# Optimization experiments

Measured on AMD Instinct MI355X. Metric: run time of the kernel, lower is better.

The kernel has to match this reference:

```python
import jax, jax.numpy as jnp
import numpy as np

N = 524288   # sparse points
C = 64       # io channels
AC = 128     # attn channels
H = 8        # heads
PS = 64      # patch size
HID = 256    # mlp hidden (mlp_ratio=2)
HD = AC // H # head dim
EPS = 1e-5


def _ln(x):
    mu = x.mean(-1, keepdims=True)
    v = x.var(-1, keepdims=True)
    return (x - mu) / jnp.sqrt(v + EPS)


def setup_inputs() -> dict:
    key = jax.random.key(0)
    ks = jax.random.split(key, 12)
    def w(k, shape, fan_in):
        return jax.random.normal(k, shape, jnp.float32) * (1.0 / np.sqrt(fan_in))
    return {
        "feats": jax.random.normal(ks[0], (N, C), jnp.float32),
        "w_pre": w(ks[1], (C, AC), C),    "b_pre": jnp.zeros((AC,), jnp.float32),
        "g1": jnp.ones((AC,), jnp.float32), "b1": jnp.zeros((AC,), jnp.float32),
        "w_qkv": w(ks[2], (AC, 3 * AC), AC), "b_qkv": jnp.zeros((3 * AC,), jnp.float32),
        "w_proj": w(ks[3], (AC, AC), AC), "b_proj": jnp.zeros((AC,), jnp.float32),
        "g2": jnp.ones((AC,), jnp.float32), "b2": jnp.zeros((AC,), jnp.float32),
        "w_m1": w(ks[4], (AC, HID), AC),  "b_m1": jnp.zeros((HID,), jnp.float32),
        "w_m2": w(ks[5], (HID, AC), HID), "b_m2": jnp.zeros((AC,), jnp.float32),
        "w_post": w(ks[6], (AC, C), AC),  "b_post": jnp.zeros((C,), jnp.float32),
    }


def reference(feats, w_pre, b_pre, g1, b1, w_qkv, b_qkv, w_proj, b_proj,
              g2, b2, w_m1, b_m1, w_m2, b_m2, w_post, b_post):
    # pre_proj: 1x1 sparse conv == pointwise linear on [N, C]
    x2 = feats @ w_pre + b_pre                            # [N, AC]
    # norm1 -> patch attention
    n1 = _ln(x2) * g1 + b1
    P = N // PS
    qkv = (n1 @ w_qkv + b_qkv).reshape(P, PS, 3, H, HD)   # patches of 64 pts
    q, k, v = qkv[:, :, 0], qkv[:, :, 1], qkv[:, :, 2]    # [P, PS, H, HD]
    scale = HD ** -0.5
    att = jnp.einsum('pqhd,pkhd->phqk', q, k) * scale     # [P, H, PS, PS]
    att = jax.nn.softmax(att, axis=-1)
    o = jnp.einsum('phqk,pkhd->pqhd', att, v).reshape(N, AC)
    h = o @ w_proj + b_proj
    x2 = x2 + h                                           # residual 1
    # norm2 -> pointwise MLP (1x1 conv -> GELU -> 1x1 conv)
    n2 = _ln(x2) * g2 + b2
    h2 = jax.nn.gelu(n2 @ w_m1 + b_m1, approximate=False) @ w_m2 + b_m2
    x2 = x2 + h2                                          # residual 2
    return x2 @ w_post + b_post                           # post_proj [N, C]
```

## Files before the change

kernel.cpp:

```cpp
#include <hip/hip_runtime.h>
#include <hip/hip_bf16.h>
#include <math.h>


typedef __bf16 bf16;
typedef __bf16 bf16x8 __attribute__((ext_vector_type(8)));
typedef __bf16 bf16x4 __attribute__((ext_vector_type(4)));
typedef float  f32x4  __attribute__((ext_vector_type(4)));

#define MFMA16(a, b, c) __builtin_amdgcn_mfma_f32_16x16x32_bf16((a), (b), (c), 0, 0, 0)

constexpr int OFF_PRE  = 0;
constexpr int OFF_QKV  = 8192;
constexpr int OFF_PROJ = 57344;
constexpr int OFF_M1   = 73728;
constexpr int OFF_M2   = 106496;
constexpr int OFF_POST = 139264;

template <int W>
__device__ __forceinline__ int swz(int row, int col) {
    constexpr int CH = W >> 3;
    constexpr int M  = (CH - 1) < 15 ? (CH - 1) : 15;
    const int c = (col >> 3) ^ (row & M);
    return row * W + c * 8 + (col & 7);
}

__device__ __forceinline__ bf16x8 zero8() {
    bf16x8 z;
#pragma unroll
    for (int j = 0; j < 8; ++j) z[j] = (bf16)0.0f;
    return z;
}

__device__ __forceinline__ void st4(bf16* p, const f32x4 v) {
    bf16x4 o;
#pragma unroll
    for (int r = 0; r < 4; ++r) o[r] = (bf16)v[r];
    *(bf16x4*)p = o;
}

__device__ __forceinline__ float gelu_f(float x) {
    const float u = 0.79788456f * x * (1.0f + 0.044715f * x * x);
    const float e = __builtin_amdgcn_exp2f(u * 2.8853900817779268f);
    return x - x * __builtin_amdgcn_rcpf(e + 1.0f);
}

__global__ void pack_all(const float* __restrict__ w_pre,
                         const float* __restrict__ w_qkv,
                         const float* __restrict__ w_proj,
                         const float* __restrict__ w_m1,
                         const float* __restrict__ w_m2,
                         const float* __restrict__ w_post,
                         bf16* __restrict__ dst) {
    const int t = blockIdx.x;
    const float* src;
    int Ncol, KT, off, t0;
    if (t < 16)       { src = w_pre;  Ncol = 128; KT = 2; off = OFF_PRE;  t0 = 0; }
    else if (t < 112) { src = w_qkv;  Ncol = 384; KT = 4; off = OFF_QKV;  t0 = 16; }
    else if (t < 144) { src = w_proj; Ncol = 128; KT = 4; off = OFF_PROJ; t0 = 112; }
    else if (t < 208) { src = w_m1;   Ncol = 256; KT = 4; off = OFF_M1;   t0 = 144; }
    else if (t < 272) { src = w_m2;   Ncol = 128; KT = 8; off = OFF_M2;   t0 = 208; }
    else              { src = w_post; Ncol = 64;  KT = 4; off = OFF_POST; t0 = 272; }
    const int tile = t - t0;
    const int lane = threadIdx.x;
    const int mt = tile / KT, kt = tile - mt * KT;
    const int n  = mt * 16 + (lane & 15);
    const int k0 = kt * 32 + (lane >> 4) * 8;
    bf16x8 v;
#pragma unroll
    for (int j = 0; j < 8; ++j) v[j] = (bf16)src[(k0 + j) * Ncol + n];
    *(bf16x8*)(dst + off + ((long)(tile * 64 + lane)) * 8) = v;
}

__device__ __forceinline__ void ln_rows(const bf16* __restrict__ in,
                                        bf16* __restrict__ outb,
                                        const float* __restrict__ g,
                                        const float* __restrict__ b, int tid) {
    const int row = tid >> 3, sub = tid & 7;
    bf16x8 c0 = *(const bf16x8*)(in + swz<128>(row, sub * 16));
    bf16x8 c1 = *(const bf16x8*)(in + swz<128>(row, sub * 16 + 8));
    float v[16];
#pragma unroll
    for (int j = 0; j < 8; ++j) { v[j] = (float)c0[j]; v[8 + j] = (float)c1[j]; }
    float s = 0.f, ss = 0.f;
#pragma unroll
    for (int j = 0; j < 16; ++j) { s += v[j]; ss += v[j] * v[j]; }
#pragma unroll
    for (int m = 1; m <= 4; m <<= 1) {
        s += __shfl_xor(s, m);
        ss += __shfl_xor(ss, m);
    }
    const float mu   = s * (1.0f / 128.0f);
    const float rstd = __builtin_amdgcn_rsqf(ss * (1.0f / 128.0f) - mu * mu + 1e-5f);
    bf16x8 o0, o1;
#pragma unroll
    for (int j = 0; j < 8; ++j) {
        o0[j] = (bf16)((v[j] - mu) * rstd * g[sub * 16 + j] + b[sub * 16 + j]);
        o1[j] = (bf16)((v[8 + j] - mu) * rstd * g[sub * 16 + 8 + j] + b[sub * 16 + 8 + j]);
    }
    *(bf16x8*)(outb + swz<128>(row, sub * 16)) = o0;
    *(bf16x8*)(outb + swz<128>(row, sub * 16 + 8)) = o1;
}

__global__ __launch_bounds__(512, 4)
void fused_block_kernel(const float* __restrict__ feats,
                        const bf16* __restrict__ wp,
                        const float* __restrict__ b_pre,
                        const float* __restrict__ g1, const float* __restrict__ b1,
                        const float* __restrict__ b_qkv,
                        const float* __restrict__ b_proj,
                        const float* __restrict__ g2, const float* __restrict__ b2,
                        const float* __restrict__ b_m1,
                        const float* __restrict__ b_m2,
                        const float* __restrict__ b_post,
                        float* __restrict__ out) {
    __shared__ __align__(16) bf16 RA[64 * 128];
    __shared__ __align__(16) bf16 RB[64 * 128];
    __shared__ __align__(16) bf16 RC[64 * 128];

    const int tid  = threadIdx.x;
    const int w    = tid >> 6;
    const int lane = tid & 63;
    const int q    = lane >> 4;
    const int l15  = lane & 15;
    const long base = (long)blockIdx.x * 64;
    const f32x4 fzero = {0.f, 0.f, 0.f, 0.f};

    {
        const int row = tid >> 3, ch = tid & 7;
        const float* src = feats + (base + row) * 64 + ch * 8;
        float4 a = *(const float4*)src;
        float4 b = *(const float4*)(src + 4);
        bf16x8 v;
        v[0] = (bf16)a.x; v[1] = (bf16)a.y; v[2] = (bf16)a.z; v[3] = (bf16)a.w;
        v[4] = (bf16)b.x; v[5] = (bf16)b.y; v[6] = (bf16)b.z; v[7] = (bf16)b.w;
        *(bf16x8*)(RA + swz<64>(row, ch * 8)) = v;
    }
    __syncthreads();

    f32x4 x2[4];

    {
        f32x4 acc[4];
#pragma unroll
        for (int tt = 0; tt < 4; ++tt) acc[tt] = fzero;
#pragma unroll
        for (int ks = 0; ks < 2; ++ks) {
            bf16x8 afr = *(const bf16x8*)(wp + OFF_PRE + ((w * 2 + ks) * 64 + lane) * 8);
#pragma unroll
            for (int tt = 0; tt < 4; ++tt) {
                bf16x8 bfr = *(const bf16x8*)(RA + swz<64>(tt * 16 + l15, ks * 32 + q * 8));
                acc[tt] = MFMA16(afr, bfr, acc[tt]);
            }
        }
        const f32x4 bias = *(const f32x4*)(b_pre + w * 16 + q * 4);
#pragma unroll
        for (int tt = 0; tt < 4; ++tt) {
#pragma unroll
            for (int r = 0; r < 4; ++r) x2[tt][r] = acc[tt][r] + bias[r];
            st4(RB + swz<128>(tt * 16 + l15, w * 16 + q * 4), x2[tt]);
        }
    }
    __syncthreads();

    ln_rows(RB, RA, g1, b1, tid);
    __syncthreads();

    {
        bf16x8 Bfr[4][4];
#pragma unroll
        for (int ks = 0; ks < 4; ++ks)
#pragma unroll
            for (int tt = 0; tt < 4; ++tt)
                Bfr[ks][tt] = *(const bf16x8*)(RA + swz<128>(tt * 16 + l15, ks * 32 + q * 8));
        __syncthreads();
#pragma unroll
        for (int part = 0; part < 3; ++part) {
            const int mt = part * 8 + w;
            f32x4 acc[4];
#pragma unroll
            for (int tt = 0; tt < 4; ++tt) acc[tt] = fzero;
#pragma unroll
            for (int ks = 0; ks < 4; ++ks) {
                bf16x8 afr = *(const bf16x8*)(wp + OFF_QKV + ((mt * 4 + ks) * 64 + lane) * 8);
#pragma unroll
                for (int tt = 0; tt < 4; ++tt) acc[tt] = MFMA16(afr, Bfr[ks][tt], acc[tt]);
            }
            const f32x4 bias = *(const f32x4*)(b_qkv + mt * 16 + q * 4);
            if (part == 0) {
#pragma unroll
                for (int tt = 0; tt < 4; ++tt)
                    st4(RA + swz<128>(tt * 16 + l15, w * 16 + q * 4), acc[tt] + bias);
            } else if (part == 1) {
#pragma unroll
                for (int tt = 0; tt < 4; ++tt)
                    st4(RB + swz<128>(tt * 16 + l15, w * 16 + q * 4), acc[tt] + bias);
            } else {
#pragma unroll
                for (int tt = 0; tt < 4; ++tt)
#pragma unroll
                    for (int r = 0; r < 4; ++r)
                        RC[w * 1024 + swz<64>(q * 4 + r, tt * 16 + l15)] =
                            (bf16)(acc[tt][r] + bias[r]);
            }
        }
    }
    __syncthreads();

    {
        const int colA = w * 16 + (q & 1) * 8;
        const bool hi = (q >= 2);
        const bf16x8 z8 = zero8();
        bf16* const slab = RC + w * 1024;
        bf16x8 Kf[4];
#pragma unroll
        for (int kt = 0; kt < 4; ++kt) {
            bf16x8 t = *(const bf16x8*)(RB + swz<128>(kt * 16 + l15, colA));
            Kf[kt] = hi ? z8 : t;
        }
        bf16x8 Vf[2];
#pragma unroll
        for (int ks = 0; ks < 2; ++ks)
            Vf[ks] = *(const bf16x8*)(slab + swz<64>(l15, ks * 32 + q * 8));
#pragma unroll
        for (int qt = 0; qt < 4; ++qt) {
            bf16x8 t = *(const bf16x8*)(RA + swz<128>(qt * 16 + l15, colA));
            bf16x8 Qf = hi ? z8 : t;
            float P[4][4];
            float lsum = 0.f;
#pragma unroll
            for (int kt = 0; kt < 4; ++kt) {
                f32x4 S = MFMA16(Kf[kt], Qf, fzero);
#pragma unroll
                for (int r = 0; r < 4; ++r) {
                    const float sv = S[r] * 0.25f;
                    const float e = __builtin_amdgcn_exp2f(sv * 1.4426950408889634f);
                    P[kt][r] = e;
                    lsum += e;
                }
            }
            lsum += __shfl_xor(lsum, 16);
            lsum += __shfl_xor(lsum, 32);
            const float inv = __builtin_amdgcn_rcpf(lsum);
#pragma unroll
            for (int kt = 0; kt < 4; ++kt) {
                f32x4 e4;
#pragma unroll
                for (int r = 0; r < 4; ++r) e4[r] = P[kt][r] * inv;
                st4(slab + swz<64>(l15, kt * 16 + q * 4), e4);
            }
            f32x4 O = fzero;
#pragma unroll
            for (int ks = 0; ks < 2; ++ks) {
                bf16x8 Bf = *(const bf16x8*)(slab + swz<64>(l15, ks * 32 + q * 8));
                O = MFMA16(Vf[ks], Bf, O);
            }
            st4(RA + swz<128>(qt * 16 + l15, w * 16 + q * 4), O);
        }
    }
    __syncthreads();

    {
        f32x4 acc[4];
#pragma unroll
        for (int tt = 0; tt < 4; ++tt) acc[tt] = fzero;
#pragma unroll
        for (int ks = 0; ks < 4; ++ks) {
            bf16x8 afr = *(const bf16x8*)(wp + OFF_PROJ + ((w * 4 + ks) * 64 + lane) * 8);
#pragma unroll
            for (int tt = 0; tt < 4; ++tt) {
                bf16x8 bfr = *(const bf16x8*)(RA + swz<128>(tt * 16 + l15, ks * 32 + q * 8));
                acc[tt] = MFMA16(afr, bfr, acc[tt]);
            }
        }
        const f32x4 bias = *(const f32x4*)(b_proj + w * 16 + q * 4);
#pragma unroll
        for (int tt = 0; tt < 4; ++tt) {
#pragma unroll
            for (int r = 0; r < 4; ++r) x2[tt][r] += acc[tt][r] + bias[r];
            st4(RB + swz<128>(tt * 16 + l15, w * 16 + q * 4), x2[tt]);
        }
    }
    __syncthreads();

    ln_rows(RB, RA, g2, b2, tid);
    __syncthreads();

    {
        bf16x8 Bfr[4][4];
#pragma unroll
        for (int ks = 0; ks < 4; ++ks)
#pragma unroll
            for (int tt = 0; tt < 4; ++tt)
                Bfr[ks][tt] = *(const bf16x8*)(RA + swz<128>(tt * 16 + l15, ks * 32 + q * 8));
#pragma unroll
        for (int half = 0; half < 2; ++half) {
            const int mt = w * 2 + half;
            f32x4 acc[4];
#pragma unroll
            for (int tt = 0; tt < 4; ++tt) acc[tt] = fzero;
#pragma unroll
            for (int ks = 0; ks < 4; ++ks) {
                bf16x8 afr = *(const bf16x8*)(wp + OFF_M1 + ((mt * 4 + ks) * 64 + lane) * 8);
#pragma unroll
                for (int tt = 0; tt < 4; ++tt) acc[tt] = MFMA16(afr, Bfr[ks][tt], acc[tt]);
            }
            const f32x4 bias = *(const f32x4*)(b_m1 + mt * 16 + q * 4);
            bf16* const dst = (mt < 8) ? RB : RC;
            const int colb  = (mt & 7) * 16 + q * 4;
#pragma unroll
            for (int tt = 0; tt < 4; ++tt) {
                f32x4 gl;
#pragma unroll
                for (int r = 0; r < 4; ++r) gl[r] = gelu_f(acc[tt][r] + bias[r]);
                st4(dst + swz<128>(tt * 16 + l15, colb), gl);
            }
        }
    }
    __syncthreads();

    {
        f32x4 acc[4];
#pragma unroll
        for (int tt = 0; tt < 4; ++tt) acc[tt] = fzero;
#pragma unroll
        for (int ks = 0; ks < 8; ++ks) {
            bf16x8 afr = *(const bf16x8*)(wp + OFF_M2 + ((w * 8 + ks) * 64 + lane) * 8);
            const bf16* const srcH = (ks < 4) ? RB : RC;
            const int colb = (ks & 3) * 32 + q * 8;
#pragma unroll
            for (int tt = 0; tt < 4; ++tt) {
                bf16x8 bfr = *(const bf16x8*)(srcH + swz<128>(tt * 16 + l15, colb));
                acc[tt] = MFMA16(afr, bfr, acc[tt]);
            }
        }
        const f32x4 bias = *(const f32x4*)(b_m2 + w * 16 + q * 4);
#pragma unroll
        for (int tt = 0; tt < 4; ++tt) {
#pragma unroll
            for (int r = 0; r < 4; ++r) x2[tt][r] += acc[tt][r] + bias[r];
            st4(RA + swz<128>(tt * 16 + l15, w * 16 + q * 4), x2[tt]);
        }
    }
    __syncthreads();

    {
        const int ct  = w >> 1;
        const int tt0 = (w & 1) * 2;
        f32x4 acc[2];
#pragma unroll
        for (int rr = 0; rr < 2; ++rr) acc[rr] = fzero;
#pragma unroll
        for (int ks = 0; ks < 4; ++ks) {
            bf16x8 afr = *(const bf16x8*)(wp + OFF_POST + ((ct * 4 + ks) * 64 + lane) * 8);
#pragma unroll
            for (int rr = 0; rr < 2; ++rr) {
                bf16x8 bfr = *(const bf16x8*)(RA + swz<128>((tt0 + rr) * 16 + l15, ks * 32 + q * 8));
                acc[rr] = MFMA16(afr, bfr, acc[rr]);
            }
        }
        const f32x4 bias = *(const f32x4*)(b_post + ct * 16 + q * 4);
#pragma unroll
        for (int rr = 0; rr < 2; ++rr) {
            f32x4 v = acc[rr] + bias;
            *(f32x4*)(out + (base + (tt0 + rr) * 16 + l15) * 64 + ct * 16 + q * 4) = v;
        }
    }
}

extern "C" void kernel_launch(void* const* d_in, const int* in_sizes, int n_in,
                              void* d_out, int out_size, void* d_ws, size_t ws_size,
                              hipStream_t stream) {
    const float* feats  = (const float*)d_in[0];
    const float* w_pre  = (const float*)d_in[1];
    const float* b_pre  = (const float*)d_in[2];
    const float* g1     = (const float*)d_in[3];
    const float* b1     = (const float*)d_in[4];
    const float* w_qkv  = (const float*)d_in[5];
    const float* b_qkv  = (const float*)d_in[6];
    const float* w_proj = (const float*)d_in[7];
    const float* b_proj = (const float*)d_in[8];
    const float* g2     = (const float*)d_in[9];
    const float* b2     = (const float*)d_in[10];
    const float* w_m1   = (const float*)d_in[11];
    const float* b_m1   = (const float*)d_in[12];
    const float* w_m2   = (const float*)d_in[13];
    const float* b_m2   = (const float*)d_in[14];
    const float* w_post = (const float*)d_in[15];
    const float* b_post = (const float*)d_in[16];

    bf16* wp = (bf16*)d_ws;

    pack_all<<<288, 64, 0, stream>>>(w_pre, w_qkv, w_proj, w_m1, w_m2, w_post, wp);

    fused_block_kernel<<<8192, 512, 0, stream>>>(
        feats, wp, b_pre, g1, b1, b_qkv, b_proj, g2, b2, b_m1, b_m2, b_post,
        (float*)d_out);
}
```

Before: 621.8 us.

## Prefetch next-stage weight fragments into registers before barriers across GEMM stages

Weight fragments for each GEMM stage (pre, qkv part 0, proj, m1, m2, post) are now loaded from global memory into registers one stage early, so their latency overlaps the previous stage's compute and the barrier. The MLP first layer is also restructured to loop over row tiles with a per-tile B fragment, replacing a 4x4 fragment array. This lowers the live-register peak there and makes room for the prefetched weights. The trade-off is higher register pressure across barriers, which could reduce occupancy or cause spills.

```diff
diff --git a/kernel.cpp b/kernel.cpp
--- a/kernel.cpp
+++ b/kernel.cpp
@@ -126,11 +126,15 @@
     const long base = (long)blockIdx.x * 64;
     const f32x4 fzero = {0.f, 0.f, 0.f, 0.f};
 
+    bf16x8 pfPRE[2];
     {
         const int row = tid >> 3, ch = tid & 7;
         const float* src = feats + (base + row) * 64 + ch * 8;
         float4 a = *(const float4*)src;
         float4 b = *(const float4*)(src + 4);
+#pragma unroll
+        for (int ks = 0; ks < 2; ++ks)
+            pfPRE[ks] = *(const bf16x8*)(wp + OFF_PRE + ((w * 2 + ks) * 64 + lane) * 8);
         bf16x8 v;
         v[0] = (bf16)a.x; v[1] = (bf16)a.y; v[2] = (bf16)a.z; v[3] = (bf16)a.w;
         v[4] = (bf16)b.x; v[5] = (bf16)b.y; v[6] = (bf16)b.z; v[7] = (bf16)b.w;
@@ -146,11 +150,10 @@
         for (int tt = 0; tt < 4; ++tt) acc[tt] = fzero;
 #pragma unroll
         for (int ks = 0; ks < 2; ++ks) {
-            bf16x8 afr = *(const bf16x8*)(wp + OFF_PRE + ((w * 2 + ks) * 64 + lane) * 8);
 #pragma unroll
             for (int tt = 0; tt < 4; ++tt) {
                 bf16x8 bfr = *(const bf16x8*)(RA + swz<64>(tt * 16 + l15, ks * 32 + q * 8));
-                acc[tt] = MFMA16(afr, bfr, acc[tt]);
+                acc[tt] = MFMA16(pfPRE[ks], bfr, acc[tt]);
             }
         }
         const f32x4 bias = *(const f32x4*)(b_pre + w * 16 + q * 4);
@@ -167,6 +170,10 @@
     __syncthreads();
 
     {
+        bf16x8 pfQ[4];
+#pragma unroll
+        for (int ks = 0; ks < 4; ++ks)
+            pfQ[ks] = *(const bf16x8*)(wp + OFF_QKV + ((w * 4 + ks) * 64 + lane) * 8);
         bf16x8 Bfr[4][4];
 #pragma unroll
         for (int ks = 0; ks < 4; ++ks)
@@ -182,7 +189,9 @@
             for (int tt = 0; tt < 4; ++tt) acc[tt] = fzero;
 #pragma unroll
             for (int ks = 0; ks < 4; ++ks) {
-                bf16x8 afr = *(const bf16x8*)(wp + OFF_QKV + ((mt * 4 + ks) * 64 + lane) * 8);
+                bf16x8 afr = (part == 0)
+                    ? pfQ[ks]
+                    : *(const bf16x8*)(wp + OFF_QKV + ((mt * 4 + ks) * 64 + lane) * 8);
 #pragma unroll
                 for (int tt = 0; tt < 4; ++tt) acc[tt] = MFMA16(afr, Bfr[ks][tt], acc[tt]);
             }
@@ -207,7 +216,11 @@
     }
     __syncthreads();
 
-    {
+    bf16x8 pfPROJ[4];
+    {
+#pragma unroll
+        for (int ks = 0; ks < 4; ++ks)
+            pfPROJ[ks] = *(const bf16x8*)(wp + OFF_PROJ + ((w * 4 + ks) * 64 + lane) * 8);
         const int colA = w * 16 + (q & 1) * 8;
         const bool hi = (q >= 2);
         const bf16x8 z8 = zero8();
@@ -260,17 +273,21 @@
     }
     __syncthreads();
 
-    {
+    bf16x8 pfM1[8];
+    {
+#pragma unroll
+        for (int kk = 0; kk < 8; ++kk)
+            pfM1[kk] = *(const bf16x8*)(wp + OFF_M1 +
+                (((w * 2 + (kk >> 2)) * 4 + (kk & 3)) * 64 + lane) * 8);
         f32x4 acc[4];
 #pragma unroll
         for (int tt = 0; tt < 4; ++tt) acc[tt] = fzero;
 #pragma unroll
         for (int ks = 0; ks < 4; ++ks) {
-            bf16x8 afr = *(const bf16x8*)(wp + OFF_PROJ + ((w * 4 + ks) * 64 + lane) * 8);
 #pragma unroll
             for (int tt = 0; tt < 4; ++tt) {
                 bf16x8 bfr = *(const bf16x8*)(RA + swz<128>(tt * 16 + l15, ks * 32 + q * 8));
-                acc[tt] = MFMA16(afr, bfr, acc[tt]);
+                acc[tt] = MFMA16(pfPROJ[ks], bfr, acc[tt]);
             }
         }
         const f32x4 bias = *(const f32x4*)(b_proj + w * 16 + q * 4);
@@ -286,52 +303,52 @@
     ln_rows(RB, RA, g2, b2, tid);
     __syncthreads();
 
-    {
-        bf16x8 Bfr[4][4];
+    bf16x8 pfM2[8];
+    {
+#pragma unroll
+        for (int tt = 0; tt < 4; ++tt) {
+            bf16x8 Bfr[4];
+#pragma unroll
+            for (int ks = 0; ks < 4; ++ks)
+                Bfr[ks] = *(const bf16x8*)(RA + swz<128>(tt * 16 + l15, ks * 32 + q * 8));
+#pragma unroll
+            for (int half = 0; half < 2; ++half) {
+                const int mt = w * 2 + half;
+                f32x4 acc = fzero;
+#pragma unroll
+                for (int ks = 0; ks < 4; ++ks)
+                    acc = MFMA16(pfM1[half * 4 + ks], Bfr[ks], acc);
+                const f32x4 bias = *(const f32x4*)(b_m1 + mt * 16 + q * 4);
+                f32x4 gl;
+#pragma unroll
+                for (int r = 0; r < 4; ++r) gl[r] = gelu_f(acc[r] + bias[r]);
+                bf16* const dst = (mt < 8) ? RB : RC;
+                st4(dst + swz<128>(tt * 16 + l15, (mt & 7) * 16 + q * 4), gl);
+            }
+        }
+#pragma unroll
+        for (int ks = 0; ks < 8; ++ks)
+            pfM2[ks] = *(const bf16x8*)(wp + OFF_M2 + ((w * 8 + ks) * 64 + lane) * 8);
+    }
+    __syncthreads();
+
+    bf16x8 pfPOST[4];
+    {
+        const int ct = w >> 1;
 #pragma unroll
         for (int ks = 0; ks < 4; ++ks)
-#pragma unroll
-            for (int tt = 0; tt < 4; ++tt)
-                Bfr[ks][tt] = *(const bf16x8*)(RA + swz<128>(tt * 16 + l15, ks * 32 + q * 8));
-#pragma unroll
-        for (int half = 0; half < 2; ++half) {
-            const int mt = w * 2 + half;
-            f32x4 acc[4];
-#pragma unroll
-            for (int tt = 0; tt < 4; ++tt) acc[tt] = fzero;
-#pragma unroll
-            for (int ks = 0; ks < 4; ++ks) {
-                bf16x8 afr = *(const bf16x8*)(wp + OFF_M1 + ((mt * 4 + ks) * 64 + lane) * 8);
-#pragma unroll
-                for (int tt = 0; tt < 4; ++tt) acc[tt] = MFMA16(afr, Bfr[ks][tt], acc[tt]);
-            }
-            const f32x4 bias = *(const f32x4*)(b_m1 + mt * 16 + q * 4);
-            bf16* const dst = (mt < 8) ? RB : RC;
-            const int colb  = (mt & 7) * 16 + q * 4;
-#pragma unroll
-            for (int tt = 0; tt < 4; ++tt) {
-                f32x4 gl;
-#pragma unroll
-                for (int r = 0; r < 4; ++r) gl[r] = gelu_f(acc[tt][r] + bias[r]);
-                st4(dst + swz<128>(tt * 16 + l15, colb), gl);
-            }
-        }
-    }
-    __syncthreads();
-
-    {
+            pfPOST[ks] = *(const bf16x8*)(wp + OFF_POST + ((ct * 4 + ks) * 64 + lane) * 8);
         f32x4 acc[4];
 #pragma unroll
         for (int tt = 0; tt < 4; ++tt) acc[tt] = fzero;
 #pragma unroll
         for (int ks = 0; ks < 8; ++ks) {
-            bf16x8 afr = *(const bf16x8*)(wp + OFF_M2 + ((w * 8 + ks) * 64 + lane) * 8);
             const bf16* const srcH = (ks < 4) ? RB : RC;
             const int colb = (ks & 3) * 32 + q * 8;
 #pragma unroll
             for (int tt = 0; tt < 4; ++tt) {
                 bf16x8 bfr = *(const bf16x8*)(srcH + swz<128>(tt * 16 + l15, colb));
-                acc[tt] = MFMA16(afr, bfr, acc[tt]);
+                acc[tt] = MFMA16(pfM2[ks], bfr, acc[tt]);
             }
         }
         const f32x4 bias = *(const f32x4*)(b_m2 + w * 16 + q * 4);
@@ -352,11 +369,10 @@
         for (int rr = 0; rr < 2; ++rr) acc[rr] = fzero;
 #pragma unroll
         for (int ks = 0; ks < 4; ++ks) {
-            bf16x8 afr = *(const bf16x8*)(wp + OFF_POST + ((ct * 4 + ks) * 64 + lane) * 8);
 #pragma unroll
             for (int rr = 0; rr < 2; ++rr) {
                 bf16x8 bfr = *(const bf16x8*)(RA + swz<128>((tt0 + rr) * 16 + l15, ks * 32 + q * 8));
-                acc[rr] = MFMA16(afr, bfr, acc[rr]);
+                acc[rr] = MFMA16(pfPOST[ks], bfr, acc[rr]);
             }
         }
         const f32x4 bias = *(const f32x4*)(b_post + ct * 16 + q * 4);
```

After: 618.9 us. No clear change (-0.5%).
